# Kernel optimization log

Hardware: AMD Instinct MI355X
Metric: run time of the kernel (lower is better)

The kernel has to match this reference:

```python
import jax, jax.numpy as jnp
from jax import lax
import numpy as np

NUM_ITER = 20
STOP_THRESH = 1e-4
NEG_SLOPE = 0.01


def _min_pool(x, window):
    # min over window == -max_pool(-x); stride 1, SAME padding matches pad=(k-1)//2
    return lax.reduce_window(x, jnp.inf, lax.min, (1, 1) + window, (1,) * 5, 'SAME')


def _max_pool(x, window):
    return lax.reduce_window(x, -jnp.inf, lax.max, (1, 1) + window, (1,) * 5, 'SAME')


def soft_erode(img):
    # kernels: (3,3,3) and (3,3,1) from anisotropy (1,1,0.5); both preserve shape
    e1 = _min_pool(img, (3, 3, 3))
    e2 = _min_pool(img, (3, 3, 1))
    return jnp.minimum(e1, e2)


def soft_dilate(img):
    return _max_pool(img, (3, 3, 3))


def soft_open(img):
    return soft_dilate(soft_erode(img))


def soft_skel(img):
    skel = jax.nn.leaky_relu(img - soft_open(img), NEG_SLOPE)
    prev = jnp.zeros_like(skel)
    active = jnp.asarray(True)

    def step(carry, _):
        cimg, cskel, cprev, cact = carry
        img2 = soft_erode(cimg)
        delta = jax.nn.leaky_relu(img2 - soft_open(img2), NEG_SLOPE)
        upd = jax.nn.leaky_relu(delta - cskel * delta, NEG_SLOPE)
        skel2 = cskel + upd
        dn = jnp.mean(jnp.abs(skel2 - cprev))
        # torch applies the update, THEN checks delta_norm and breaks; so the
        # update is applied whenever we were active entering the iteration.
        img_n = jnp.where(cact, img2, cimg)
        skel_n = jnp.where(cact, skel2, cskel)
        prev_n = jnp.where(cact, skel2, cprev)
        act_n = cact & (dn >= STOP_THRESH)
        return (img_n, skel_n, prev_n, act_n), None

    (_, skel, _, _), _ = lax.scan(step, (img, skel, prev, active), None, length=NUM_ITER)
    return skel


def setup_inputs() -> dict:
    key = jax.random.key(0)
    img = jax.random.uniform(key, (2, 1, 128, 256, 256), dtype=jnp.float32)
    return {"img": img}


def reference(img):
    # distance_transform returns zeros -> sigmoid(0)=0.5 path is absent since the
    # attribute is never set in __init__; forward is just soft_skel.
    return soft_skel(img)
```

## Files before the change

### kernel.cpp

```cpp
#include <hip/hip_runtime.h>
#include <math.h>

#define D_DIM 128
#define H_DIM 256
#define W_DIM 256
#define HW (H_DIM * W_DIM)
#define HW4 (HW / 4)
#define NIMG 2
#define NPI (D_DIM * HW)
#define NTOT (NIMG * NPI)

#define TDZ 16
#define TH 16
#define TW 64

#define AW4R 18
#define AW4 19
#define AH 20
#define EW4R 17
#define EW4 19
#define EH 18

#define NLOADLIN (AH * AW4)
#define NLOADP 384
#define NERO  (EH * EW4R)
#define NOUT  (TH * (TW/4))

#define NUM_ITER 20
#define STOP_THRESH 1e-4

__device__ __forceinline__ float min3f(float a, float b, float c) { return fminf(fminf(a, b), c); }
__device__ __forceinline__ float max3f(float a, float b, float c) { return fmaxf(fmaxf(a, b), c); }
__device__ __forceinline__ float leaky(float x) { return fmaxf(x, 0.01f * x); }

#define BAR_FULL() do { asm volatile("s_waitcnt vmcnt(0) lgkmcnt(0)" ::: "memory"); \
                        __builtin_amdgcn_s_barrier(); \
                        __builtin_amdgcn_sched_barrier(0); } while (0)
#define BAR_VM2()  do { asm volatile("s_waitcnt vmcnt(2) lgkmcnt(0)" ::: "memory"); \
                        __builtin_amdgcn_s_barrier(); \
                        __builtin_amdgcn_sched_barrier(0); } while (0)
#define BAR_VM1()  do { asm volatile("s_waitcnt vmcnt(1) lgkmcnt(0)" ::: "memory"); \
                        __builtin_amdgcn_s_barrier(); \
                        __builtin_amdgcn_sched_barrier(0); } while (0)
#define BAR_LDS() do { asm volatile("s_waitcnt lgkmcnt(0)" ::: "memory"); \
                       __builtin_amdgcn_s_barrier(); \
                       __builtin_amdgcn_sched_barrier(0); } while (0)

#define GLOAD_LDS(gp, lp) \
    __builtin_amdgcn_global_load_lds((const __attribute__((address_space(1))) unsigned int*)(gp), \
                                     (__attribute__((address_space(3))) unsigned int*)(lp), 16, 0, 0)

__global__ void init_slots(double* slots) {
    int t = threadIdx.x;
    if (t < 32) slots[t] = 0.0;
    if (t >= 32 && t < 36) ((float*)(slots + 32))[t - 32] = INFINITY;
}

__global__ __launch_bounds__(256) void skel_step(
    const float* __restrict__ a_in,
    float* __restrict__ a_out,
    float* __restrict__ skel,
    double* __restrict__ slots,
    int step)
{
    __shared__ float4 aS4[2][NLOADP];
    __shared__ float4 eT4[EH * EW4];
    __shared__ float wsum[4];
    __shared__ int s_active;

    const int t = threadIdx.x;

    if (t == 0) {
        int act = 1;
        for (int j = 1; j < step; ++j)
            if (!(slots[j] >= STOP_THRESH * (double)NTOT)) { act = 0; break; }
        s_active = act;
    }
    __syncthreads();
    if (!s_active) return;

    const float* infp = (const float*)(slots + 32);

    const int lid = blockIdx.x + 4 * (blockIdx.y + 16 * blockIdx.z);
    const int swz = (lid & 7) * 128 + (lid >> 3);
    const int bx = swz & 3;
    const int by = (swz >> 2) & 15;
    const int zz = swz >> 6;
    const int bz = zz & 7, img = zz >> 3;
    const int x0 = bx * TW, y0 = by * TH, z0 = bz * TDZ;

    const float* in = a_in + (size_t)img * NPI;
    float4* aout4 = (float4*)(a_out + (size_t)img * NPI);
    float4* sk4 = (float4*)(skel + (size_t)img * NPI);

    int lOff0; bool lVal0;
    {
        int lr = t / AW4, lc = t - lr * AW4;
        int gy = y0 - 2 + lr, gx = x0 - 4 + 4 * lc;
        lVal0 = (lc < AW4R) && ((unsigned)gy < H_DIM) && ((unsigned)gx <= (unsigned)(W_DIM - 4));
        lOff0 = gy * W_DIM + gx;
    }
    const bool hasL1 = t < 128;
    int lOff1 = 0; bool lVal1 = false;
    if (hasL1) {
        int q = t + 256;
        int lr = q / AW4, lc = q - lr * AW4;
        int gy = y0 - 2 + lr, gx = x0 - 4 + 4 * lc;
        lVal1 = (q < NLOADLIN) && (lc < AW4R) && ((unsigned)gy < H_DIM)
                && ((unsigned)gx <= (unsigned)(W_DIM - 4));
        lOff1 = gy * W_DIM + gx;
    }
    const int wbase = (t >> 6) << 6;

    int eRd0, eWr0; bool sA0, sB0, sC0, sD0;
    {
        int mh = t / EW4R, ej = t - mh * EW4R;
        eRd0 = mh * AW4 + ej;
        eWr0 = mh * EW4 + ej;
        int gy = y0 - 1 + mh;
        bool gok = (unsigned)gy < H_DIM;
        int gxb = x0 - 2 + 4 * ej;
        sA0 = gok && ((unsigned)(gxb + 0) < W_DIM);
        sB0 = gok && ((unsigned)(gxb + 1) < W_DIM);
        sC0 = gok && ((unsigned)(gxb + 2) < W_DIM);
        sD0 = gok && ((unsigned)(gxb + 3) < W_DIM);
    }
    const bool hasE1 = t < (NERO - 256);
    int eRd1 = 0, eWr1 = 0; bool sA1 = false, sB1 = false, sC1 = false, sD1 = false;
    if (hasE1) {
        int q = t + 256;
        int mh = q / EW4R, ej = q - mh * EW4R;
        eRd1 = mh * AW4 + ej;
        eWr1 = mh * EW4 + ej;
        int gy = y0 - 1 + mh;
        bool gok = (unsigned)gy < H_DIM;
        int gxb = x0 - 2 + 4 * ej;
        sA1 = gok && ((unsigned)(gxb + 0) < W_DIM);
        sB1 = gok && ((unsigned)(gxb + 1) < W_DIM);
        sC1 = gok && ((unsigned)(gxb + 2) < W_DIM);
        sD1 = gok && ((unsigned)(gxb + 3) < W_DIM);
    }

    const int oh = t >> 4, wq = t & 15;
    const int oRd = oh * EW4 + wq;
    const int oAc = (oh + 2) * AW4 + wq + 1;
    size_t ob = ((size_t)z0 * HW + (size_t)(y0 + oh) * W_DIM + (size_t)x0) / 4 + wq;

    const float INF = INFINITY;
    const float4 inf4 = make_float4(INF, INF, INF, INF);
    const float4 ninf4 = make_float4(-INF, -INF, -INF, -INF);
    float4 m0P2 = inf4, m0P1 = inf4, m1P2 = inf4, m1P1 = inf4;
    float4 xP2 = ninf4, xP1 = ninf4;
    float4 acA = make_float4(0, 0, 0, 0), acB = acA, ecA = acA;
    float lsum = 0.f;

    {
        int z = z0 - 2;
        bool zok = (unsigned)z < D_DIM;
        const float* p = in + (size_t)z * HW;
        const float* s0 = (zok && lVal0) ? (p + lOff0) : infp;
        GLOAD_LDS(s0, &aS4[0][wbase]);
        if (hasL1) {
            const float* s1 = (zok && lVal1) ? (p + lOff1) : infp;
            GLOAD_LDS(s1, &aS4[0][256 + wbase]);
        }
    }

    for (int i = 0; i < TDZ + 4; ++i) {
        const int cur = i & 1;

        if (i < 5) { BAR_FULL(); }
        else if (step == NUM_ITER) { BAR_VM1(); }
        else { BAR_VM2(); }

        float4 ggPre;
        if (step > 0 && i >= 4) ggPre = sk4[ob];
        __builtin_amdgcn_sched_barrier(0);

        if (i <= TDZ + 2) {
            int z = z0 - 1 + i;
            bool zok = (unsigned)z < D_DIM;
            const float* p = in + (size_t)z * HW;
            const float* s0 = (zok && lVal0) ? (p + lOff0) : infp;
            GLOAD_LDS(s0, &aS4[cur ^ 1][wbase]);
            if (hasL1) {
                const float* s1 = (zok && lVal1) ? (p + lOff1) : infp;
                GLOAD_LDS(s1, &aS4[cur ^ 1][256 + wbase]);
            }
        }
        __builtin_amdgcn_sched_barrier(0);

        const bool zp = (unsigned)(z0 - 3 + i) < D_DIM;

        {
            const float4* s = aS4[cur];
            float4 a0 = s[eRd0],           b0 = s[eRd0 + 1];
            float4 a1 = s[eRd0 + AW4],     b1 = s[eRd0 + AW4 + 1];
            float4 a2 = s[eRd0 + 2 * AW4], b2 = s[eRd0 + 2 * AW4 + 1];
            float4 va, vb, mC;
            va.x = min3f(a0.x, a1.x, a2.x);
            va.y = min3f(a0.y, a1.y, a2.y);
            va.z = min3f(a0.z, a1.z, a2.z);
            va.w = min3f(a0.w, a1.w, a2.w);
            vb.x = min3f(b0.x, b1.x, b2.x);
            vb.y = min3f(b0.y, b1.y, b2.y);
            vb.z = min3f(b0.z, b1.z, b2.z);
            mC.x = min3f(va.y, va.z, va.w);
            mC.y = min3f(va.z, va.w, vb.x);
            mC.z = min3f(va.w, vb.x, vb.y);
            mC.w = min3f(vb.x, vb.y, vb.z);
            if (i >= 2 && zp) {
                float4 e;
                e.x = sA0 ? min3f(m0P2.x, m0P1.x, mC.x) : -INF;
                e.y = sB0 ? min3f(m0P2.y, m0P1.y, mC.y) : -INF;
                e.z = sC0 ? min3f(m0P2.z, m0P1.z, mC.z) : -INF;
                e.w = sD0 ? min3f(m0P2.w, m0P1.w, mC.w) : -INF;
                eT4[eWr0] = e;
            }
            m0P2 = m0P1; m0P1 = mC;
        }
        if (hasE1) {
            const float4* s = aS4[cur];
            float4 a0 = s[eRd1],           b0 = s[eRd1 + 1];
            float4 a1 = s[eRd1 + AW4],     b1 = s[eRd1 + AW4 + 1];
            float4 a2 = s[eRd1 + 2 * AW4], b2 = s[eRd1 + 2 * AW4 + 1];
            float4 va, vb, mC;
            va.x = min3f(a0.x, a1.x, a2.x);
            va.y = min3f(a0.y, a1.y, a2.y);
            va.z = min3f(a0.z, a1.z, a2.z);
            va.w = min3f(a0.w, a1.w, a2.w);
            vb.x = min3f(b0.x, b1.x, b2.x);
            vb.y = min3f(b0.y, b1.y, b2.y);
            vb.z = min3f(b0.z, b1.z, b2.z);
            mC.x = min3f(va.y, va.z, va.w);
            mC.y = min3f(va.z, va.w, vb.x);
            mC.z = min3f(va.w, vb.x, vb.y);
            mC.w = min3f(vb.x, vb.y, vb.z);
            if (i >= 2 && zp) {
                float4 e;
                e.x = sA1 ? min3f(m1P2.x, m1P1.x, mC.x) : -INF;
                e.y = sB1 ? min3f(m1P2.y, m1P1.y, mC.y) : -INF;
                e.z = sC1 ? min3f(m1P2.z, m1P1.z, mC.z) : -INF;
                e.w = sD1 ? min3f(m1P2.w, m1P1.w, mC.w) : -INF;
                eT4[eWr1] = e;
            }
            m1P2 = m1P1; m1P1 = mC;
        }

        BAR_LDS();

        {
            const float4 aCn = aS4[cur][oAc];
            float4 xC, ecB;
            if (i >= 2 && zp) {
                float4 A0 = eT4[oRd],           B0 = eT4[oRd + 1];
                float4 A1 = eT4[oRd + EW4],     B1 = eT4[oRd + EW4 + 1];
                float4 A2 = eT4[oRd + 2 * EW4], B2 = eT4[oRd + 2 * EW4 + 1];
                float4 va, vb;
                va.x = max3f(A0.x, A1.x, A2.x);
                va.y = max3f(A0.y, A1.y, A2.y);
                va.z = max3f(A0.z, A1.z, A2.z);
                va.w = max3f(A0.w, A1.w, A2.w);
                vb.x = max3f(B0.x, B1.x, B2.x);
                vb.y = max3f(B0.y, B1.y, B2.y);
                vb.z = max3f(B0.z, B1.z, B2.z);
                xC.x = max3f(va.y, va.z, va.w);
                xC.y = max3f(va.z, va.w, vb.x);
                xC.z = max3f(va.w, vb.x, vb.y);
                xC.w = max3f(vb.x, vb.y, vb.z);
                ecB.x = A1.z; ecB.y = A1.w; ecB.z = B1.x; ecB.w = B1.y;
            } else {
                xC = ninf4; ecB = ninf4;
            }

            if (i >= 4) {
                float4 dl;
                dl.x = leaky(acA.x - max3f(xP2.x, xP1.x, xC.x));
                dl.y = leaky(acA.y - max3f(xP2.y, xP1.y, xC.y));
                dl.z = leaky(acA.z - max3f(xP2.z, xP1.z, xC.z));
                dl.w = leaky(acA.w - max3f(xP2.w, xP1.w, xC.w));
                if (step < NUM_ITER) aout4[ob] = ecA;
                if (step == 0) {
                    sk4[ob] = dl;
                } else {
                    float4 gg = ggPre;
                    float4 up, gn;
                    up.x = leaky(dl.x - gg.x * dl.x); gn.x = gg.x + up.x;
                    up.y = leaky(dl.y - gg.y * dl.y); gn.y = gg.y + up.y;
                    up.z = leaky(dl.z - gg.z * dl.z); gn.z = gg.z + up.z;
                    up.w = leaky(dl.w - gg.w * dl.w); gn.w = gg.w + up.w;
                    sk4[ob] = gn;
                    if (step == 1)
                        lsum += fabsf(gn.x) + fabsf(gn.y) + fabsf(gn.z) + fabsf(gn.w);
                    else
                        lsum += fabsf(up.x) + fabsf(up.y) + fabsf(up.z) + fabsf(up.w);
                }
                ob += HW4;
            }
            xP2 = xP1; xP1 = xC;
            acA = acB; acB = aCn;
            ecA = ecB;
        }
    }

    if (step > 0) {
        #pragma unroll
        for (int off = 32; off > 0; off >>= 1)
            lsum += __shfl_down(lsum, off, 64);
        const int lane = t & 63, wid = t >> 6;
        if (lane == 0) wsum[wid] = lsum;
        __syncthreads();
        if (t == 0) {
            float b = wsum[0] + wsum[1] + wsum[2] + wsum[3];
            atomicAdd(&slots[step], (double)b);
        }
    }
}

extern "C" void kernel_launch(void* const* d_in, const int* in_sizes, int n_in,
                              void* d_out, int out_size, void* d_ws, size_t ws_size,
                              hipStream_t stream) {
    const float* img = (const float*)d_in[0];
    float* out = (float*)d_out;
    float* buf0 = (float*)d_ws;
    float* buf1 = buf0 + NTOT;
    double* slots = (double*)(buf1 + NTOT);

    init_slots<<<1, 64, 0, stream>>>(slots);

    dim3 grid(W_DIM / TW, H_DIM / TH, (D_DIM / TDZ) * NIMG);
    for (int s = 0; s <= NUM_ITER; ++s) {
        const float* ain = (s == 0) ? img : ((s & 1) ? buf0 : buf1);
        float* aout = (s & 1) ? buf1 : buf0;
        skel_step<<<grid, 256, 0, stream>>>(ain, aout, out, slots, s);
    }
}
```

Baseline: 387.1 us.

## Process two z-slices per barrier round with quad-buffered LDS staging

Restructures the z-sweep so that each loop iteration handles two slices. The input staging buffer grows to four LDS slots and the erosion tile to two, so only half as many block barriers are needed and two slices of loads stay in flight (vmcnt 4/2). The aim is to cut barrier and synchronisation overhead and deepen the prefetch, at the cost of more LDS per block, which may lower occupancy, and more register pressure.

```diff
diff --git a/kernel.cpp b/kernel.cpp
--- a/kernel.cpp
+++ b/kernel.cpp
@@ -36,10 +36,10 @@
 #define BAR_FULL() do { asm volatile("s_waitcnt vmcnt(0) lgkmcnt(0)" ::: "memory"); \
                         __builtin_amdgcn_s_barrier(); \
                         __builtin_amdgcn_sched_barrier(0); } while (0)
-#define BAR_VM2()  do { asm volatile("s_waitcnt vmcnt(2) lgkmcnt(0)" ::: "memory"); \
+#define BAR_VM4()  do { asm volatile("s_waitcnt vmcnt(4) lgkmcnt(0)" ::: "memory"); \
                         __builtin_amdgcn_s_barrier(); \
                         __builtin_amdgcn_sched_barrier(0); } while (0)
-#define BAR_VM1()  do { asm volatile("s_waitcnt vmcnt(1) lgkmcnt(0)" ::: "memory"); \
+#define BAR_VM2()  do { asm volatile("s_waitcnt vmcnt(2) lgkmcnt(0)" ::: "memory"); \
                         __builtin_amdgcn_s_barrier(); \
                         __builtin_amdgcn_sched_barrier(0); } while (0)
 #define BAR_LDS() do { asm volatile("s_waitcnt lgkmcnt(0)" ::: "memory"); \
@@ -63,8 +63,8 @@
     double* __restrict__ slots,
     int step)
 {
-    __shared__ float4 aS4[2][NLOADP];
-    __shared__ float4 eT4[EH * EW4];
+    __shared__ float4 aS4[4][NLOADP];
+    __shared__ float4 eT4[2][EH * EW4];
     __shared__ float wsum[4];
     __shared__ int s_active;
 
@@ -147,161 +147,185 @@
     size_t ob = ((size_t)z0 * HW + (size_t)(y0 + oh) * W_DIM + (size_t)x0) / 4 + wq;
 
     const float INF = INFINITY;
+    const float4 ninf4 = make_float4(-INF, -INF, -INF, -INF);
     const float4 inf4 = make_float4(INF, INF, INF, INF);
-    const float4 ninf4 = make_float4(-INF, -INF, -INF, -INF);
     float4 m0P2 = inf4, m0P1 = inf4, m1P2 = inf4, m1P1 = inf4;
     float4 xP2 = ninf4, xP1 = ninf4;
-    float4 acA = make_float4(0, 0, 0, 0), acB = acA, ecA = acA;
+    float4 acP2 = make_float4(0, 0, 0, 0), acP1 = acP2, ecP = acP2;
     float lsum = 0.f;
 
-    {
-        int z = z0 - 2;
+    for (int s = 0; s < 2; ++s) {
+        int z = z0 - 2 + s;
         bool zok = (unsigned)z < D_DIM;
         const float* p = in + (size_t)z * HW;
         const float* s0 = (zok && lVal0) ? (p + lOff0) : infp;
-        GLOAD_LDS(s0, &aS4[0][wbase]);
+        GLOAD_LDS(s0, &aS4[s][wbase]);
         if (hasL1) {
             const float* s1 = (zok && lVal1) ? (p + lOff1) : infp;
-            GLOAD_LDS(s1, &aS4[0][256 + wbase]);
+            GLOAD_LDS(s1, &aS4[s][256 + wbase]);
         }
     }
 
-    for (int i = 0; i < TDZ + 4; ++i) {
-        const int cur = i & 1;
-
-        if (i < 5) { BAR_FULL(); }
-        else if (step == NUM_ITER) { BAR_VM1(); }
-        else { BAR_VM2(); }
-
-        float4 ggPre;
-        if (step > 0 && i >= 4) ggPre = sk4[ob];
+    #define ERODE_SLICE(SLOT, ZPV, DO_E, ETI, mP2v, mP1v, m1P2v, m1P1v)            \
+    do {                                                                           \
+        const float4* s_ = aS4[SLOT];                                              \
+        float4 a0 = s_[eRd0],           b0 = s_[eRd0 + 1];                         \
+        float4 a1 = s_[eRd0 + AW4],     b1 = s_[eRd0 + AW4 + 1];                   \
+        float4 a2 = s_[eRd0 + 2 * AW4], b2 = s_[eRd0 + 2 * AW4 + 1];               \
+        float4 va, vb, mC;                                                         \
+        va.x = min3f(a0.x, a1.x, a2.x); va.y = min3f(a0.y, a1.y, a2.y);            \
+        va.z = min3f(a0.z, a1.z, a2.z); va.w = min3f(a0.w, a1.w, a2.w);            \
+        vb.x = min3f(b0.x, b1.x, b2.x); vb.y = min3f(b0.y, b1.y, b2.y);            \
+        vb.z = min3f(b0.z, b1.z, b2.z);                                            \
+        mC.x = min3f(va.y, va.z, va.w); mC.y = min3f(va.z, va.w, vb.x);            \
+        mC.z = min3f(va.w, vb.x, vb.y); mC.w = min3f(vb.x, vb.y, vb.z);            \
+        if ((DO_E) && (ZPV)) {                                                     \
+            float4 e;                                                              \
+            e.x = sA0 ? min3f(mP2v.x, mP1v.x, mC.x) : -INF;                        \
+            e.y = sB0 ? min3f(mP2v.y, mP1v.y, mC.y) : -INF;                        \
+            e.z = sC0 ? min3f(mP2v.z, mP1v.z, mC.z) : -INF;                        \
+            e.w = sD0 ? min3f(mP2v.w, mP1v.w, mC.w) : -INF;                        \
+            eT4[ETI][eWr0] = e;                                                    \
+        }                                                                          \
+        mP2v = mP1v; mP1v = mC;                                                    \
+        if (hasE1) {                                                               \
+            float4 c0 = s_[eRd1],           d0 = s_[eRd1 + 1];                     \
+            float4 c1 = s_[eRd1 + AW4],     d1 = s_[eRd1 + AW4 + 1];               \
+            float4 c2 = s_[eRd1 + 2 * AW4], d2 = s_[eRd1 + 2 * AW4 + 1];           \
+            float4 wa, wb, nC;                                                     \
+            wa.x = min3f(c0.x, c1.x, c2.x); wa.y = min3f(c0.y, c1.y, c2.y);        \
+            wa.z = min3f(c0.z, c1.z, c2.z); wa.w = min3f(c0.w, c1.w, c2.w);        \
+            wb.x = min3f(d0.x, d1.x, d2.x); wb.y = min3f(d0.y, d1.y, d2.y);        \
+            wb.z = min3f(d0.z, d1.z, d2.z);                                        \
+            nC.x = min3f(wa.y, wa.z, wa.w); nC.y = min3f(wa.z, wa.w, wb.x);        \
+            nC.z = min3f(wa.w, wb.x, wb.y); nC.w = min3f(wb.x, wb.y, wb.z);        \
+            if ((DO_E) && (ZPV)) {                                                 \
+                float4 e;                                                          \
+                e.x = sA1 ? min3f(m1P2v.x, m1P1v.x, nC.x) : -INF;                  \
+                e.y = sB1 ? min3f(m1P2v.y, m1P1v.y, nC.y) : -INF;                  \
+                e.z = sC1 ? min3f(m1P2v.z, m1P1v.z, nC.z) : -INF;                  \
+                e.w = sD1 ? min3f(m1P2v.w, m1P1v.w, nC.w) : -INF;                  \
+                eT4[ETI][eWr1] = e;                                                \
+            }                                                                      \
+            m1P2v = m1P1v; m1P1v = nC;                                             \
+        }                                                                          \
+    } while (0)
+
+    #define MAX9(ETI, xCv, ecv)                                                    \
+    do {                                                                           \
+        const float4* eP_ = eT4[ETI];                                              \
+        float4 A0 = eP_[oRd],           B0 = eP_[oRd + 1];                         \
+        float4 A1 = eP_[oRd + EW4],     B1 = eP_[oRd + EW4 + 1];                   \
+        float4 A2 = eP_[oRd + 2 * EW4], B2 = eP_[oRd + 2 * EW4 + 1];               \
+        float4 va, vb;                                                             \
+        va.x = max3f(A0.x, A1.x, A2.x); va.y = max3f(A0.y, A1.y, A2.y);            \
+        va.z = max3f(A0.z, A1.z, A2.z); va.w = max3f(A0.w, A1.w, A2.w);            \
+        vb.x = max3f(B0.x, B1.x, B2.x); vb.y = max3f(B0.y, B1.y, B2.y);            \
+        vb.z = max3f(B0.z, B1.z, B2.z);                                            \
+        xCv.x = max3f(va.y, va.z, va.w); xCv.y = max3f(va.z, va.w, vb.x);          \
+        xCv.z = max3f(va.w, vb.x, vb.y); xCv.w = max3f(vb.x, vb.y, vb.z);          \
+        ecv.x = A1.z; ecv.y = A1.w; ecv.z = B1.x; ecv.w = B1.y;                    \
+    } while (0)
+
+    for (int k = 0; k < (TDZ + 4) / 2; ++k) {
+        const int i0 = 2 * k, i1 = 2 * k + 1;
+        const int slot0 = i0 & 3, slot1 = i1 & 3;
+
+        if (k < 3) { BAR_FULL(); }
+        else if (step == NUM_ITER) { BAR_VM2(); }
+        else { BAR_VM4(); }
+
+        float4 ggPre0, ggPre1;
+        if (step > 0 && i0 >= 4) { ggPre0 = sk4[ob]; ggPre1 = sk4[ob + HW4]; }
         __builtin_amdgcn_sched_barrier(0);
 
-        if (i <= TDZ + 2) {
-            int z = z0 - 1 + i;
-            bool zok = (unsigned)z < D_DIM;
-            const float* p = in + (size_t)z * HW;
-            const float* s0 = (zok && lVal0) ? (p + lOff0) : infp;
-            GLOAD_LDS(s0, &aS4[cur ^ 1][wbase]);
-            if (hasL1) {
-                const float* s1 = (zok && lVal1) ? (p + lOff1) : infp;
-                GLOAD_LDS(s1, &aS4[cur ^ 1][256 + wbase]);
+        if (k <= (TDZ + 4) / 2 - 2) {
+            for (int s = 0; s < 2; ++s) {
+                int z = z0 + 2 * k + s;
+                bool zok = (unsigned)z < D_DIM;
+                const float* p = in + (size_t)z * HW;
+                const float* s0 = (zok && lVal0) ? (p + lOff0) : infp;
+                GLOAD_LDS(s0, &aS4[(i0 + 2 + s) & 3][wbase]);
+                if (hasL1) {
+                    const float* s1 = (zok && lVal1) ? (p + lOff1) : infp;
+                    GLOAD_LDS(s1, &aS4[(i0 + 2 + s) & 3][256 + wbase]);
+                }
             }
         }
         __builtin_amdgcn_sched_barrier(0);
 
-        const bool zp = (unsigned)(z0 - 3 + i) < D_DIM;
+        const bool zp0 = (unsigned)(z0 - 3 + i0) < D_DIM;
+        const bool zp1 = (unsigned)(z0 - 3 + i1) < D_DIM;
+        const bool doE = (i0 >= 2);
+
+        ERODE_SLICE(slot0, zp0, doE, 0, m0P2, m0P1, m1P2, m1P1);
+        ERODE_SLICE(slot1, zp1, (i1 >= 2), 1, m0P2, m0P1, m1P2, m1P1);
+
+        const float4 aCn0 = aS4[slot0][oAc];
+        const float4 aCn1 = aS4[slot1][oAc];
+
+        BAR_LDS();
 
         {
-            const float4* s = aS4[cur];
-            float4 a0 = s[eRd0],           b0 = s[eRd0 + 1];
-            float4 a1 = s[eRd0 + AW4],     b1 = s[eRd0 + AW4 + 1];
-            float4 a2 = s[eRd0 + 2 * AW4], b2 = s[eRd0 + 2 * AW4 + 1];
-            float4 va, vb, mC;
-            va.x = min3f(a0.x, a1.x, a2.x);
-            va.y = min3f(a0.y, a1.y, a2.y);
-            va.z = min3f(a0.z, a1.z, a2.z);
-            va.w = min3f(a0.w, a1.w, a2.w);
-            vb.x = min3f(b0.x, b1.x, b2.x);
-            vb.y = min3f(b0.y, b1.y, b2.y);
-            vb.z = min3f(b0.z, b1.z, b2.z);
-            mC.x = min3f(va.y, va.z, va.w);
-            mC.y = min3f(va.z, va.w, vb.x);
-            mC.z = min3f(va.w, vb.x, vb.y);
-            mC.w = min3f(vb.x, vb.y, vb.z);
-            if (i >= 2 && zp) {
-                float4 e;
-                e.x = sA0 ? min3f(m0P2.x, m0P1.x, mC.x) : -INF;
-                e.y = sB0 ? min3f(m0P2.y, m0P1.y, mC.y) : -INF;
-                e.z = sC0 ? min3f(m0P2.z, m0P1.z, mC.z) : -INF;
-                e.w = sD0 ? min3f(m0P2.w, m0P1.w, mC.w) : -INF;
-                eT4[eWr0] = e;
+            float4 xC0, ecB0, xC1, ecB1;
+            if (doE && zp0) { MAX9(0, xC0, ecB0); } else { xC0 = ninf4; ecB0 = ninf4; }
+            if (doE && zp1) { MAX9(1, xC1, ecB1); } else { xC1 = ninf4; ecB1 = ninf4; }
+
+            if (i0 >= 4) {
+                {
+                    float4 dl;
+                    dl.x = leaky(acP2.x - max3f(xP2.x, xP1.x, xC0.x));
+                    dl.y = leaky(acP2.y - max3f(xP2.y, xP1.y, xC0.y));
+                    dl.z = leaky(acP2.z - max3f(xP2.z, xP1.z, xC0.z));
+                    dl.w = leaky(acP2.w - max3f(xP2.w, xP1.w, xC0.w));
+                    if (step < NUM_ITER) aout4[ob] = ecP;
+                    if (step == 0) {
+                        sk4[ob] = dl;
+                    } else {
+                        float4 gg = ggPre0, up, gn;
+                        up.x = leaky(dl.x - gg.x * dl.x); gn.x = gg.x + up.x;
+                        up.y = leaky(dl.y - gg.y * dl.y); gn.y = gg.y + up.y;
+                        up.z = leaky(dl.z - gg.z * dl.z); gn.z = gg.z + up.z;
+                        up.w = leaky(dl.w - gg.w * dl.w); gn.w = gg.w + up.w;
+                        sk4[ob] = gn;
+                        if (step == 1)
+                            lsum += fabsf(gn.x) + fabsf(gn.y) + fabsf(gn.z) + fabsf(gn.w);
+                        else
+                            lsum += fabsf(up.x) + fabsf(up.y) + fabsf(up.z) + fabsf(up.w);
+                    }
+                }
+                {
+                    float4 dl;
+                    dl.x = leaky(acP1.x - max3f(xP1.x, xC0.x, xC1.x));
+                    dl.y = leaky(acP1.y - max3f(xP1.y, xC0.y, xC1.y));
+                    dl.z = leaky(acP1.z - max3f(xP1.z, xC0.z, xC1.z));
+                    dl.w = leaky(acP1.w - max3f(xP1.w, xC0.w, xC1.w));
+                    if (step < NUM_ITER) aout4[ob + HW4] = ecB0;
+                    if (step == 0) {
+                        sk4[ob + HW4] = dl;
+                    } else {
+                        float4 gg = ggPre1, up, gn;
+                        up.x = leaky(dl.x - gg.x * dl.x); gn.x = gg.x + up.x;
+                        up.y = leaky(dl.y - gg.y * dl.y); gn.y = gg.y + up.y;
+                        up.z = leaky(dl.z - gg.z * dl.z); gn.z = gg.z + up.z;
+                        up.w = leaky(dl.w - gg.w * dl.w); gn.w = gg.w + up.w;
+                        sk4[ob + HW4] = gn;
+                        if (step == 1)
+                            lsum += fabsf(gn.x) + fabsf(gn.y) + fabsf(gn.z) + fabsf(gn.w);
+                        else
+                            lsum += fabsf(up.x) + fabsf(up.y) + fabsf(up.z) + fabsf(up.w);
+                    }
+                }
+                ob += 2 * HW4;
             }
-            m0P2 = m0P1; m0P1 = mC;
+            xP2 = xC0; xP1 = xC1;
+            acP2 = aCn0; acP1 = aCn1;
+            ecP = ecB1;
         }
-        if (hasE1) {
-            const float4* s = aS4[cur];
-            float4 a0 = s[eRd1],           b0 = s[eRd1 + 1];
-            float4 a1 = s[eRd1 + AW4],     b1 = s[eRd1 + AW4 + 1];
-            float4 a2 = s[eRd1 + 2 * AW4], b2 = s[eRd1 + 2 * AW4 + 1];
-            float4 va, vb, mC;
-            va.x = min3f(a0.x, a1.x, a2.x);
-            va.y = min3f(a0.y, a1.y, a2.y);
-            va.z = min3f(a0.z, a1.z, a2.z);
-            va.w = min3f(a0.w, a1.w, a2.w);
-            vb.x = min3f(b0.x, b1.x, b2.x);
-            vb.y = min3f(b0.y, b1.y, b2.y);
-            vb.z = min3f(b0.z, b1.z, b2.z);
-            mC.x = min3f(va.y, va.z, va.w);
-            mC.y = min3f(va.z, va.w, vb.x);
-            mC.z = min3f(va.w, vb.x, vb.y);
-            mC.w = min3f(vb.x, vb.y, vb.z);
-            if (i >= 2 && zp) {
-                float4 e;
-                e.x = sA1 ? min3f(m1P2.x, m1P1.x, mC.x) : -INF;
-                e.y = sB1 ? min3f(m1P2.y, m1P1.y, mC.y) : -INF;
-                e.z = sC1 ? min3f(m1P2.z, m1P1.z, mC.z) : -INF;
-                e.w = sD1 ? min3f(m1P2.w, m1P1.w, mC.w) : -INF;
-                eT4[eWr1] = e;
-            }
-            m1P2 = m1P1; m1P1 = mC;
-        }
-
-        BAR_LDS();
-
-        {
-            const float4 aCn = aS4[cur][oAc];
-            float4 xC, ecB;
-            if (i >= 2 && zp) {
-                float4 A0 = eT4[oRd],           B0 = eT4[oRd + 1];
-                float4 A1 = eT4[oRd + EW4],     B1 = eT4[oRd + EW4 + 1];
-                float4 A2 = eT4[oRd + 2 * EW4], B2 = eT4[oRd + 2 * EW4 + 1];
-                float4 va, vb;
-                va.x = max3f(A0.x, A1.x, A2.x);
-                va.y = max3f(A0.y, A1.y, A2.y);
-                va.z = max3f(A0.z, A1.z, A2.z);
-                va.w = max3f(A0.w, A1.w, A2.w);
-                vb.x = max3f(B0.x, B1.x, B2.x);
-                vb.y = max3f(B0.y, B1.y, B2.y);
-                vb.z = max3f(B0.z, B1.z, B2.z);
-                xC.x = max3f(va.y, va.z, va.w);
-                xC.y = max3f(va.z, va.w, vb.x);
-                xC.z = max3f(va.w, vb.x, vb.y);
-                xC.w = max3f(vb.x, vb.y, vb.z);
-                ecB.x = A1.z; ecB.y = A1.w; ecB.z = B1.x; ecB.w = B1.y;
-            } else {
-                xC = ninf4; ecB = ninf4;
-            }
-
-            if (i >= 4) {
-                float4 dl;
-                dl.x = leaky(acA.x - max3f(xP2.x, xP1.x, xC.x));
-                dl.y = leaky(acA.y - max3f(xP2.y, xP1.y, xC.y));
-                dl.z = leaky(acA.z - max3f(xP2.z, xP1.z, xC.z));
-                dl.w = leaky(acA.w - max3f(xP2.w, xP1.w, xC.w));
-                if (step < NUM_ITER) aout4[ob] = ecA;
-                if (step == 0) {
-                    sk4[ob] = dl;
-                } else {
-                    float4 gg = ggPre;
-                    float4 up, gn;
-                    up.x = leaky(dl.x - gg.x * dl.x); gn.x = gg.x + up.x;
-                    up.y = leaky(dl.y - gg.y * dl.y); gn.y = gg.y + up.y;
-                    up.z = leaky(dl.z - gg.z * dl.z); gn.z = gg.z + up.z;
-                    up.w = leaky(dl.w - gg.w * dl.w); gn.w = gg.w + up.w;
-                    sk4[ob] = gn;
-                    if (step == 1)
-                        lsum += fabsf(gn.x) + fabsf(gn.y) + fabsf(gn.z) + fabsf(gn.w);
-                    else
-                        lsum += fabsf(up.x) + fabsf(up.y) + fabsf(up.z) + fabsf(up.w);
-                }
-                ob += HW4;
-            }
-            xP2 = xP1; xP1 = xC;
-            acA = acB; acB = aCn;
-            ecA = ecB;
-        }
-    }
+    }
+
+    #undef ERODE_SLICE
+    #undef MAX9
 
     if (step > 0) {
         #pragma unroll
```

Measured after the change: 383.4 us. About the same (-1.0%).
